# Kernel tuning notes

Measured on AMD Instinct MI355X. Metric: run time of the kernel, lower is better.

## Reference

```python
import jax, jax.numpy as jnp
import numpy as np

N, E, F_IN, H, D, C = 50000, 800000, 128, 4, 64, 40
HD = H * D
NEG_SLOPE = 0.2


def setup_inputs() -> dict:
    key = jax.random.key(0)
    ks = jax.random.split(key, 16)
    x = jax.random.normal(ks[0], (N, F_IN), dtype=jnp.float32)
    edge_index = jax.random.randint(ks[1], (2, E), 0, N, dtype=jnp.int64)
    def glorot(k, shape):
        fan = shape[0] + shape[-1]
        return jax.random.normal(k, shape, dtype=jnp.float32) * jnp.sqrt(2.0 / fan)
    params = {
        'W1': glorot(ks[2], (F_IN, HD)), 'as1': glorot(ks[3], (H, D)), 'ad1': glorot(ks[4], (H, D)), 'b1': jnp.zeros((HD,), jnp.float32),
        'W2': glorot(ks[5], (HD, HD)),   'as2': glorot(ks[6], (H, D)), 'ad2': glorot(ks[7], (H, D)), 'b2': jnp.zeros((HD,), jnp.float32),
        'W3': glorot(ks[8], (HD, HD)),   'as3': glorot(ks[9], (H, D)), 'ad3': glorot(ks[10], (H, D)), 'b3': jnp.zeros((HD,), jnp.float32),
        'Wl': glorot(ks[11], (HD, C)),   'bl': jnp.zeros((C,), jnp.float32),
    }
    return {'x': x, 'edge_index': edge_index, **params}


def gat_layer(x, src, dst, W, a_src, a_dst, b):
    # x: [N, F] -> h: [N, H, D]
    h = (x @ W).reshape(N, H, D)
    alpha_s = jnp.sum(h * a_src, axis=-1)  # [N, H]
    alpha_d = jnp.sum(h * a_dst, axis=-1)  # [N, H]
    e = alpha_s[src] + alpha_d[dst]        # [E', H]
    e = jnp.where(e > 0, e, NEG_SLOPE * e)  # leaky_relu
    # segment softmax over destination nodes
    m = jax.ops.segment_max(e, dst, num_segments=N)  # [N, H]
    m = jnp.where(jnp.isfinite(m), m, 0.0)
    ex = jnp.exp(e - m[dst])
    s = jax.ops.segment_sum(ex, dst, num_segments=N)  # [N, H]
    att = ex / (s[dst] + 1e-16)                        # [E', H]
    # weighted scatter-aggregate of source features
    out = jax.ops.segment_sum(h[src] * att[:, :, None], dst, num_segments=N)  # [N, H, D]
    return out.reshape(N, HD) + b


def reference(x, edge_index, W1, as1, ad1, b1, W2, as2, ad2, b2, W3, as3, ad3, b3, Wl, bl):
    # PyG GATConv adds self-loops by default
    loops = jnp.arange(N, dtype=edge_index.dtype)
    src = jnp.concatenate([edge_index[0], loops])
    dst = jnp.concatenate([edge_index[1], loops])
    # dropout is identity in eval mode
    h = jax.nn.elu(gat_layer(x, src, dst, W1, as1, ad1, b1))
    h = jax.nn.elu(gat_layer(h, src, dst, W2, as2, ad2, b2))
    h = jax.nn.elu(gat_layer(h, src, dst, W3, as3, ad3, b3))
    logits = h @ Wl + bl
    return jax.nn.log_softmax(logits, axis=1)
```

## Files before the change

kernel.cpp:

```cpp
#include <hip/hip_runtime.h>
#include <math.h>

#define NN 50000
#define NE 800000
#define ET (NE + NN)
#define FIN 128
#define HDIM 256
#define NHEAD 4
#define NCLS 40
#define NEG 0.2f
#define NB_SCAN ((NN + 255) / 256)

typedef short bf16x8 __attribute__((ext_vector_type(8)));
typedef float f32x4 __attribute__((ext_vector_type(4)));

__device__ __forceinline__ unsigned short f2b(float f) {
    unsigned int u = __float_as_uint(f);
    unsigned int r = (u + 0x7fffu + ((u >> 16) & 1u)) >> 16;
    return (unsigned short)r;
}
__device__ __forceinline__ float b2f(unsigned short u) {
    unsigned int x = ((unsigned int)u) << 16;
    return __uint_as_float(x);
}

__global__ void detect_kernel(const int* __restrict__ ei32, int* __restrict__ flag) {
    if (threadIdx.x == 0 && blockIdx.x == 0) {
        int is64 = 1;
        for (int i = 1; i < 256; i += 2)
            if (ei32[i] != 0) { is64 = 0; break; }
        *flag = is64;
    }
}

__device__ __forceinline__ int load_node(const int* ei32, int is64, long long idx) {
    return is64 ? ei32[2 * idx] : ei32[idx];
}

__global__ void deg_kernel(const int* __restrict__ ei32, const int* __restrict__ flag,
                           int* __restrict__ deg) {
    int e = blockIdx.x * blockDim.x + threadIdx.x;
    if (e >= ET) return;
    int is64 = *flag;
    int d = (e < NE) ? load_node(ei32, is64, (long long)NE + e) : (e - NE);
    atomicAdd(&deg[d], 1);
}

__global__ void scan1(const int* __restrict__ deg, int* __restrict__ incl,
                      int* __restrict__ bsum) {
    __shared__ int sm[256];
    int i = blockIdx.x * 256 + threadIdx.x;
    int v = (i < NN) ? deg[i] : 0;
    sm[threadIdx.x] = v;
    __syncthreads();
    for (int o = 1; o < 256; o <<= 1) {
        int add = (threadIdx.x >= o) ? sm[threadIdx.x - o] : 0;
        __syncthreads();
        sm[threadIdx.x] += add;
        __syncthreads();
    }
    if (i < NN) incl[i] = sm[threadIdx.x];
    if (threadIdx.x == 255) bsum[blockIdx.x] = sm[255];
}

__global__ void scan2(int* __restrict__ bsum) {
    __shared__ int sm[256];
    int t = threadIdx.x;
    sm[t] = (t < NB_SCAN) ? bsum[t] : 0;
    __syncthreads();
    if (t == 0) {
        int run = 0;
        for (int b = 0; b < NB_SCAN; b++) { int v = sm[b]; sm[b] = run; run += v; }
    }
    __syncthreads();
    if (t < NB_SCAN) bsum[t] = sm[t];
}

__global__ void scan3(const int* __restrict__ incl, const int* __restrict__ bsum,
                      const int* __restrict__ deg, int* __restrict__ indptr,
                      int* __restrict__ cursor) {
    int i = blockIdx.x * 256 + threadIdx.x;
    if (i < NN) {
        int v = bsum[blockIdx.x] + incl[i];
        indptr[i + 1] = v;
        cursor[i] = v - deg[i];
    }
    if (i == 0) indptr[0] = 0;
}

__global__ void fill_kernel(const int* __restrict__ ei32, const int* __restrict__ flag,
                            int* __restrict__ cursor, int* __restrict__ esrc) {
    int e = blockIdx.x * blockDim.x + threadIdx.x;
    if (e >= ET) return;
    int is64 = *flag;
    int s, d;
    if (e < NE) {
        s = load_node(ei32, is64, (long long)e);
        d = load_node(ei32, is64, (long long)NE + e);
    } else {
        s = d = e - NE;
    }
    int pos = atomicAdd(&cursor[d], 1);
    esrc[pos] = s;
}

__global__ __launch_bounds__(256) void conv_kernel(const float* __restrict__ in,
                                                   unsigned short* __restrict__ out, int n) {
    int i = (blockIdx.x * 256 + threadIdx.x) * 8;
    if (i + 8 > n) return;
    float4 f0 = *(const float4*)(in + i);
    float4 f1 = *(const float4*)(in + i + 4);
    ushort4 a, b;
    a.x = f2b(f0.x); a.y = f2b(f0.y); a.z = f2b(f0.z); a.w = f2b(f0.w);
    b.x = f2b(f1.x); b.y = f2b(f1.y); b.z = f2b(f1.z); b.w = f2b(f1.w);
    *(ushort4*)(out + i) = a;
    *(ushort4*)(out + i + 4) = b;
}

__global__ __launch_bounds__(256) void wconv_kernel(const float* __restrict__ W,
                                                    unsigned short* __restrict__ Wt, int K) {
    __shared__ float sm[32][33];
    int tx = threadIdx.x & 31, ty = threadIdx.x >> 5;
    int n0 = blockIdx.x * 32, k0 = blockIdx.y * 32;
#pragma unroll
    for (int j = 0; j < 4; j++)
        sm[ty + j * 8][tx] = W[(size_t)(k0 + ty + j * 8) * HDIM + n0 + tx];
    __syncthreads();
#pragma unroll
    for (int j = 0; j < 4; j++)
        Wt[(size_t)(n0 + ty + j * 8) * K + k0 + tx] = f2b(sm[tx][ty + j * 8]);
}

__global__ __launch_bounds__(256) void gemm_mfma(const unsigned short* __restrict__ A,
                                                 const unsigned short* __restrict__ Bt,
                                                 unsigned short* __restrict__ Cb,
                                                 const float* __restrict__ a_s,
                                                 const float* __restrict__ a_d,
                                                 float* __restrict__ als,
                                                 float* __restrict__ ald,
                                                 int M, int K) {
    __shared__ unsigned short As[128][72];
    __shared__ unsigned short Bs[64][72];
    int t = threadIdx.x;
    int lane = t & 63, wid = t >> 6;
    int r0 = blockIdx.y * 128, n0 = blockIdx.x * 64;

    f32x4 acc[2][4];
#pragma unroll
    for (int m = 0; m < 2; m++)
#pragma unroll
        for (int n = 0; n < 4; n++)
            acc[m][n] = (f32x4){0.f, 0.f, 0.f, 0.f};

    int ar = t >> 1, ah = (t & 1) * 32;
    int arow = r0 + ar; if (arow > M - 1) arow = M - 1;
    const unsigned short* ga = A + (size_t)arow * K + ah;
    int bn = t >> 2, bq = (t & 3) * 16;
    const unsigned short* gb = Bt + (size_t)(n0 + bn) * K + bq;

    int fr = lane & 15;
    int kf = (lane >> 4) * 8;

    for (int k0 = 0; k0 < K; k0 += 64) {
#pragma unroll
        for (int j = 0; j < 4; j++)
            *(uint4*)&As[ar][ah + j * 8] = *(const uint4*)(ga + k0 + j * 8);
#pragma unroll
        for (int j = 0; j < 2; j++)
            *(uint4*)&Bs[bn][bq + j * 8] = *(const uint4*)(gb + k0 + j * 8);
        __syncthreads();
#pragma unroll
        for (int kk = 0; kk < 64; kk += 32) {
            bf16x8 a[2], b[4];
#pragma unroll
            for (int m = 0; m < 2; m++)
                a[m] = *(const bf16x8*)&As[wid * 32 + m * 16 + fr][kk + kf];
#pragma unroll
            for (int n = 0; n < 4; n++)
                b[n] = *(const bf16x8*)&Bs[n * 16 + fr][kk + kf];
#pragma unroll
            for (int m = 0; m < 2; m++)
#pragma unroll
                for (int n = 0; n < 4; n++)
                    acc[m][n] = __builtin_amdgcn_mfma_f32_16x16x32_bf16(a[m], b[n], acc[m][n], 0, 0, 0);
        }
        __syncthreads();
    }

    int rbase = r0 + wid * 32 + (lane >> 4) * 4;
    int cbase = n0 + fr;
    int head = n0 >> 6;
    float asv[4], adv[4];
#pragma unroll
    for (int n = 0; n < 4; n++) {
        asv[n] = a_s[cbase + n * 16];
        adv[n] = a_d[cbase + n * 16];
    }
#pragma unroll
    for (int m = 0; m < 2; m++)
#pragma unroll
        for (int q = 0; q < 4; q++) {
            int gr = rbase + m * 16 + q;
            float vs = 0.f, vd = 0.f;
#pragma unroll
            for (int n = 0; n < 4; n++) {
                float v = acc[m][n][q];
                vs += v * asv[n];
                vd += v * adv[n];
                if (gr < M) Cb[(size_t)gr * HDIM + cbase + n * 16] = f2b(v);
            }
#pragma unroll
            for (int o = 8; o > 0; o >>= 1) {
                vs += __shfl_xor(vs, o);
                vd += __shfl_xor(vd, o);
            }
            if (fr == 0 && gr < M) {
                als[gr * NHEAD + head] = vs;
                ald[gr * NHEAD + head] = vd;
            }
        }
}

__global__ __launch_bounds__(256) void agg_kernel(const unsigned short* __restrict__ projb,
                                                  const float* __restrict__ als,
                                                  const float* __restrict__ ald,
                                                  const int* __restrict__ indptr,
                                                  const int* __restrict__ esrc,
                                                  const float* __restrict__ bias,
                                                  unsigned short* __restrict__ featb) {
    int wid = threadIdx.x >> 6;
    int v = blockIdx.x * 4 + wid;
    if (v >= NN) return;
    int lane = threadIdx.x & 63;
    int h = lane >> 4;
    int sub = lane & 15;
    int beg = indptr[v], end = indptr[v + 1];
    float adv = ald[v * NHEAD + h];

    float m = -INFINITY, ss = 0.f;
    for (int i = beg + sub; i < end; i += 16) {
        int s = esrc[i];
        float e = als[s * NHEAD + h] + adv;
        e = e > 0.f ? e : NEG * e;
        if (e > m) {
            ss = ss * __expf(m - e) + 1.f;
            m = e;
        } else {
            ss += __expf(e - m);
        }
    }
#pragma unroll
    for (int o = 8; o > 0; o >>= 1) {
        float m2 = __shfl_xor(m, o);
        float s2 = __shfl_xor(ss, o);
        float mn = fmaxf(m, m2);
        float a = (m == mn) ? ss : ss * __expf(m - mn);
        float b = (m2 == mn) ? s2 : s2 * __expf(m2 - mn);
        m = mn;
        ss = a + b;
    }
    float inv = 1.f / (ss + 1e-16f);

    float4 acc = make_float4(0.f, 0.f, 0.f, 0.f);
    int c = beg;
    for (; c + 16 <= end; c += 16) {
        int sreg = esrc[c + sub];
        float e = als[sreg * NHEAD + h] + adv;
        e = e > 0.f ? e : NEG * e;
        float wreg = __expf(e - m) * inv;

        ushort4 p[16];
#pragma unroll
        for (int j = 0; j < 16; j++) {
            int s = __shfl(sreg, j);
            p[j] = *(const ushort4*)(projb + (size_t)s * HDIM + (lane << 2));
        }
#pragma unroll
        for (int j = 0; j < 16; j++) {
            float w = __shfl(wreg, (h << 4) | j);
            acc.x += b2f(p[j].x) * w;
            acc.y += b2f(p[j].y) * w;
            acc.z += b2f(p[j].z) * w;
            acc.w += b2f(p[j].w) * w;
        }
    }
    int n = end - c;
    if (n > 0) {
        float wreg = 0.f;
        int sreg = 0;
        if (sub < n) {
            sreg = esrc[c + sub];
            float e = als[sreg * NHEAD + h] + adv;
            e = e > 0.f ? e : NEG * e;
            wreg = __expf(e - m) * inv;
        }
        for (int j = 0; j < n; j++) {
            float w = __shfl(wreg, (h << 4) | j);
            int s = __shfl(sreg, j);
            const ushort4 p = *(const ushort4*)(projb + (size_t)s * HDIM + (lane << 2));
            acc.x += b2f(p.x) * w;
            acc.y += b2f(p.y) * w;
            acc.z += b2f(p.z) * w;
            acc.w += b2f(p.w) * w;
        }
    }

    const float4 b4 = *(const float4*)(bias + (lane << 2));
    float4 r;
    r.x = acc.x + b4.x;
    r.y = acc.y + b4.y;
    r.z = acc.z + b4.z;
    r.w = acc.w + b4.w;
    r.x = r.x > 0.f ? r.x : __expf(r.x) - 1.f;
    r.y = r.y > 0.f ? r.y : __expf(r.y) - 1.f;
    r.z = r.z > 0.f ? r.z : __expf(r.z) - 1.f;
    r.w = r.w > 0.f ? r.w : __expf(r.w) - 1.f;
    ushort4 o4;
    o4.x = f2b(r.x); o4.y = f2b(r.y); o4.z = f2b(r.z); o4.w = f2b(r.w);
    *(ushort4*)(featb + (size_t)v * HDIM + (lane << 2)) = o4;
}

__global__ __launch_bounds__(256) void final_kernel(const unsigned short* __restrict__ featb,
                                                    const float* __restrict__ Wl,
                                                    const float* __restrict__ bl,
                                                    float* __restrict__ out) {
    const int BK = 16;
    __shared__ float As[BK][65];
    __shared__ float Bs[BK][65];
    int tx = threadIdx.x & 15, ty = threadIdx.x >> 4;
    int row0 = blockIdx.x * 64;
    float acc[4][4] = {};
    for (int k0 = 0; k0 < HDIM; k0 += BK) {
#pragma unroll
        for (int i = 0; i < 4; i++) {
            int l = threadIdx.x + 256 * i;
            int r = l >> 4, c = l & 15;
            int gr = row0 + r;
            float v = 0.f;
            if (gr < NN) v = b2f(featb[(size_t)gr * HDIM + k0 + c]);
            As[c][r] = v;
        }
#pragma unroll
        for (int i = 0; i < 4; i++) {
            int l = threadIdx.x + 256 * i;
            int r = l >> 6, c = l & 63;
            Bs[r][c] = (c < NCLS) ? Wl[(size_t)(k0 + r) * NCLS + c] : 0.f;
        }
        __syncthreads();
#pragma unroll
        for (int k = 0; k < BK; k++) {
            float a[4], b[4];
#pragma unroll
            for (int i = 0; i < 4; i++) a[i] = As[k][ty + 16 * i];
#pragma unroll
            for (int j = 0; j < 4; j++) b[j] = Bs[k][tx + 16 * j];
#pragma unroll
            for (int i = 0; i < 4; i++)
#pragma unroll
                for (int j = 0; j < 4; j++) acc[i][j] += a[i] * b[j];
        }
        __syncthreads();
    }
    float b0 = bl[tx], b1 = bl[tx + 16], b2 = (tx < 8) ? bl[tx + 32] : 0.f;
#pragma unroll
    for (int i = 0; i < 4; i++) {
        int gr = row0 + ty + 16 * i;
        if (gr >= NN) continue;
        float l0 = acc[i][0] + b0;
        float l1 = acc[i][1] + b1;
        float l2 = (tx < 8) ? acc[i][2] + b2 : -INFINITY;
        float m = fmaxf(fmaxf(l0, l1), l2);
#pragma unroll
        for (int o = 8; o > 0; o >>= 1) m = fmaxf(m, __shfl_xor(m, o));
        float s = __expf(l0 - m) + __expf(l1 - m) + ((tx < 8) ? __expf(l2 - m) : 0.f);
#pragma unroll
        for (int o = 8; o > 0; o >>= 1) s += __shfl_xor(s, o);
        float lse = m + __logf(s);
        out[(size_t)gr * NCLS + tx] = l0 - lse;
        out[(size_t)gr * NCLS + tx + 16] = l1 - lse;
        if (tx < 8) out[(size_t)gr * NCLS + tx + 32] = l2 - lse;
    }
}

extern "C" void kernel_launch(void* const* d_in, const int* in_sizes, int n_in,
                              void* d_out, int out_size, void* d_ws, size_t ws_size,
                              hipStream_t stream) {
    const float* x  = (const float*)d_in[0];
    const int* ei32 = (const int*)d_in[1];
    const float* W1 = (const float*)d_in[2];
    const float* as1 = (const float*)d_in[3];
    const float* ad1 = (const float*)d_in[4];
    const float* b1 = (const float*)d_in[5];
    const float* W2 = (const float*)d_in[6];
    const float* as2 = (const float*)d_in[7];
    const float* ad2 = (const float*)d_in[8];
    const float* b2 = (const float*)d_in[9];
    const float* W3 = (const float*)d_in[10];
    const float* as3 = (const float*)d_in[11];
    const float* ad3 = (const float*)d_in[12];
    const float* b3 = (const float*)d_in[13];
    const float* Wl = (const float*)d_in[14];
    const float* bl = (const float*)d_in[15];
    float* out = (float*)d_out;

    char* w = (char*)d_ws;
    unsigned short* projb = (unsigned short*)w;  w += (size_t)NN * HDIM * 2;
    unsigned short* featb = (unsigned short*)w;  w += (size_t)NN * HDIM * 2;
    unsigned short* xb    = (unsigned short*)w;  w += (size_t)NN * FIN * 2;
    unsigned short* Wt1b  = (unsigned short*)w;  w += (size_t)HDIM * FIN * 2;
    unsigned short* Wt2b  = (unsigned short*)w;  w += (size_t)HDIM * HDIM * 2;
    unsigned short* Wt3b  = (unsigned short*)w;  w += (size_t)HDIM * HDIM * 2;
    float* als  = (float*)w;  w += (size_t)NN * NHEAD * 4;
    float* ald  = (float*)w;  w += (size_t)NN * NHEAD * 4;
    int* deg    = (int*)w;    w += (size_t)NN * 4;
    int* incl   = (int*)w;    w += (size_t)NN * 4;
    int* bsum   = (int*)w;    w += 256 * 4;
    int* indptr = (int*)w;    w += (size_t)(NN + 1) * 4;
    int* cursor = (int*)w;    w += (size_t)NN * 4;
    int* esrc   = (int*)w;    w += (size_t)ET * 4;
    int* flag   = (int*)w;    w += 64;

    conv_kernel<<<(NN * FIN / 8 + 255) / 256, 256, 0, stream>>>(x, xb, NN * FIN);
    wconv_kernel<<<dim3(8, FIN / 32), 256, 0, stream>>>(W1, Wt1b, FIN);
    wconv_kernel<<<dim3(8, HDIM / 32), 256, 0, stream>>>(W2, Wt2b, HDIM);
    wconv_kernel<<<dim3(8, HDIM / 32), 256, 0, stream>>>(W3, Wt3b, HDIM);

    hipMemsetAsync(deg, 0, (size_t)NN * 4, stream);
    detect_kernel<<<1, 64, 0, stream>>>(ei32, flag);
    deg_kernel<<<(ET + 255) / 256, 256, 0, stream>>>(ei32, flag, deg);
    scan1<<<NB_SCAN, 256, 0, stream>>>(deg, incl, bsum);
    scan2<<<1, 256, 0, stream>>>(bsum);
    scan3<<<NB_SCAN, 256, 0, stream>>>(incl, bsum, deg, indptr, cursor);
    fill_kernel<<<(ET + 255) / 256, 256, 0, stream>>>(ei32, flag, cursor, esrc);

    dim3 ggrid(HDIM / 64, (NN + 127) / 128);
    int agrid = (NN + 3) / 4;

    gemm_mfma<<<ggrid, 256, 0, stream>>>(xb, Wt1b, projb, as1, ad1, als, ald, NN, FIN);
    agg_kernel<<<agrid, 256, 0, stream>>>(projb, als, ald, indptr, esrc, b1, featb);
    gemm_mfma<<<ggrid, 256, 0, stream>>>(featb, Wt2b, projb, as2, ad2, als, ald, NN, HDIM);
    agg_kernel<<<agrid, 256, 0, stream>>>(projb, als, ald, indptr, esrc, b2, featb);
    gemm_mfma<<<ggrid, 256, 0, stream>>>(featb, Wt3b, projb, as3, ad3, als, ald, NN, HDIM);
    agg_kernel<<<agrid, 256, 0, stream>>>(projb, als, ald, indptr, esrc, b3, featb);
    final_kernel<<<(NN + 63) / 64, 256, 0, stream>>>(featb, Wl, bl, out);
}
```

Measured before the change: 479.1 us.

## Fuse input bf16 conversion into GEMM, stage C via LDS, cache edge scores

```diff
diff --git a/kernel.cpp b/kernel.cpp
--- a/kernel.cpp
+++ b/kernel.cpp
@@ -104,19 +104,6 @@
     esrc[pos] = s;
 }
 
-__global__ __launch_bounds__(256) void conv_kernel(const float* __restrict__ in,
-                                                   unsigned short* __restrict__ out, int n) {
-    int i = (blockIdx.x * 256 + threadIdx.x) * 8;
-    if (i + 8 > n) return;
-    float4 f0 = *(const float4*)(in + i);
-    float4 f1 = *(const float4*)(in + i + 4);
-    ushort4 a, b;
-    a.x = f2b(f0.x); a.y = f2b(f0.y); a.z = f2b(f0.z); a.w = f2b(f0.w);
-    b.x = f2b(f1.x); b.y = f2b(f1.y); b.z = f2b(f1.z); b.w = f2b(f1.w);
-    *(ushort4*)(out + i) = a;
-    *(ushort4*)(out + i + 4) = b;
-}
-
 __global__ __launch_bounds__(256) void wconv_kernel(const float* __restrict__ W,
                                                     unsigned short* __restrict__ Wt, int K) {
     __shared__ float sm[32][33];
@@ -132,6 +119,7 @@
 }
 
 __global__ __launch_bounds__(256) void gemm_mfma(const unsigned short* __restrict__ A,
+                                                 const float* __restrict__ A32,
                                                  const unsigned short* __restrict__ Bt,
                                                  unsigned short* __restrict__ Cb,
                                                  const float* __restrict__ a_s,
@@ -155,6 +143,7 @@
     int ar = t >> 1, ah = (t & 1) * 32;
     int arow = r0 + ar; if (arow > M - 1) arow = M - 1;
     const unsigned short* ga = A + (size_t)arow * K + ah;
+    const float* ga32 = A32 ? (A32 + (size_t)arow * K + ah) : (const float*)0;
     int bn = t >> 2, bq = (t & 3) * 16;
     const unsigned short* gb = Bt + (size_t)(n0 + bn) * K + bq;
 
@@ -162,9 +151,23 @@
     int kf = (lane >> 4) * 8;
 
     for (int k0 = 0; k0 < K; k0 += 64) {
-#pragma unroll
-        for (int j = 0; j < 4; j++)
-            *(uint4*)&As[ar][ah + j * 8] = *(const uint4*)(ga + k0 + j * 8);
+        if (A32) {
+#pragma unroll
+            for (int j = 0; j < 4; j++) {
+                float4 fa = *(const float4*)(ga32 + k0 + j * 8);
+                float4 fb = *(const float4*)(ga32 + k0 + j * 8 + 4);
+                union { ushort4 u[2]; uint4 v; } pk;
+                pk.u[0].x = f2b(fa.x); pk.u[0].y = f2b(fa.y);
+                pk.u[0].z = f2b(fa.z); pk.u[0].w = f2b(fa.w);
+                pk.u[1].x = f2b(fb.x); pk.u[1].y = f2b(fb.y);
+                pk.u[1].z = f2b(fb.z); pk.u[1].w = f2b(fb.w);
+                *(uint4*)&As[ar][ah + j * 8] = pk.v;
+            }
+        } else {
+#pragma unroll
+            for (int j = 0; j < 4; j++)
+                *(uint4*)&As[ar][ah + j * 8] = *(const uint4*)(ga + k0 + j * 8);
+        }
 #pragma unroll
         for (int j = 0; j < 2; j++)
             *(uint4*)&Bs[bn][bq + j * 8] = *(const uint4*)(gb + k0 + j * 8);
@@ -207,7 +210,6 @@
                 float v = acc[m][n][q];
                 vs += v * asv[n];
                 vd += v * adv[n];
-                if (gr < M) Cb[(size_t)gr * HDIM + cbase + n * 16] = f2b(v);
             }
 #pragma unroll
             for (int o = 8; o > 0; o >>= 1) {
@@ -219,6 +221,25 @@
                 ald[gr * NHEAD + head] = vd;
             }
         }
+
+    unsigned short (*Cs)[68] = (unsigned short(*)[68])&As[0][0];
+    int lr0 = wid * 32 + (lane >> 4) * 4;
+#pragma unroll
+    for (int m = 0; m < 2; m++)
+#pragma unroll
+        for (int q = 0; q < 4; q++)
+#pragma unroll
+            for (int n = 0; n < 4; n++)
+                Cs[lr0 + m * 16 + q][fr + n * 16] = f2b(acc[m][n][q]);
+    __syncthreads();
+    int tr = t >> 4;
+    int tc = (t & 15) * 4;
+#pragma unroll
+    for (int rr = 0; rr < 8; rr++) {
+        int lr = tr + rr * 16;
+        int gr = r0 + lr;
+        if (gr < M) *(ushort4*)(Cb + (size_t)gr * HDIM + n0 + tc) = *(const ushort4*)&Cs[lr][tc];
+    }
 }
 
 __global__ __launch_bounds__(256) void agg_kernel(const unsigned short* __restrict__ projb,
@@ -237,11 +258,16 @@
     int beg = indptr[v], end = indptr[v + 1];
     float adv = ald[v * NHEAD + h];
 
+    float e0 = 0.f, e1 = 0.f;
+    int s0r = 0, s1r = 0;
     float m = -INFINITY, ss = 0.f;
-    for (int i = beg + sub; i < end; i += 16) {
+    int idx = 0;
+    for (int i = beg + sub; i < end; i += 16, idx++) {
         int s = esrc[i];
         float e = als[s * NHEAD + h] + adv;
         e = e > 0.f ? e : NEG * e;
+        if (idx == 0) { e0 = e; s0r = s; }
+        else if (idx == 1) { e1 = e; s1r = s; }
         if (e > m) {
             ss = ss * __expf(m - e) + 1.f;
             m = e;
@@ -263,11 +289,18 @@
 
     float4 acc = make_float4(0.f, 0.f, 0.f, 0.f);
     int c = beg;
-    for (; c + 16 <= end; c += 16) {
-        int sreg = esrc[c + sub];
-        float e = als[sreg * NHEAD + h] + adv;
-        e = e > 0.f ? e : NEG * e;
-        float wreg = __expf(e - m) * inv;
+    int chunk = 0;
+    for (; c + 16 <= end; c += 16, chunk++) {
+        int sreg;
+        float eC;
+        if (chunk == 0) { sreg = s0r; eC = e0; }
+        else if (chunk == 1) { sreg = s1r; eC = e1; }
+        else {
+            sreg = esrc[c + sub];
+            eC = als[sreg * NHEAD + h] + adv;
+            eC = eC > 0.f ? eC : NEG * eC;
+        }
+        float wreg = __expf(eC - m) * inv;
 
         ushort4 p[16];
 #pragma unroll
@@ -286,14 +319,16 @@
     }
     int n = end - c;
     if (n > 0) {
-        float wreg = 0.f;
-        int sreg = 0;
-        if (sub < n) {
-            sreg = esrc[c + sub];
-            float e = als[sreg * NHEAD + h] + adv;
-            e = e > 0.f ? e : NEG * e;
-            wreg = __expf(e - m) * inv;
-        }
+        int sreg;
+        float eT;
+        if (chunk == 0) { sreg = s0r; eT = e0; }
+        else if (chunk == 1) { sreg = s1r; eT = e1; }
+        else {
+            sreg = (sub < n) ? esrc[c + sub] : 0;
+            eT = als[sreg * NHEAD + h] + adv;
+            eT = eT > 0.f ? eT : NEG * eT;
+        }
+        float wreg = (sub < n) ? __expf(eT - m) * inv : 0.f;
         for (int j = 0; j < n; j++) {
             float w = __shfl(wreg, (h << 4) | j);
             int s = __shfl(sreg, j);
@@ -406,7 +441,6 @@
     char* w = (char*)d_ws;
     unsigned short* projb = (unsigned short*)w;  w += (size_t)NN * HDIM * 2;
     unsigned short* featb = (unsigned short*)w;  w += (size_t)NN * HDIM * 2;
-    unsigned short* xb    = (unsigned short*)w;  w += (size_t)NN * FIN * 2;
     unsigned short* Wt1b  = (unsigned short*)w;  w += (size_t)HDIM * FIN * 2;
     unsigned short* Wt2b  = (unsigned short*)w;  w += (size_t)HDIM * HDIM * 2;
     unsigned short* Wt3b  = (unsigned short*)w;  w += (size_t)HDIM * HDIM * 2;
@@ -420,7 +454,6 @@
     int* esrc   = (int*)w;    w += (size_t)ET * 4;
     int* flag   = (int*)w;    w += 64;
 
-    conv_kernel<<<(NN * FIN / 8 + 255) / 256, 256, 0, stream>>>(x, xb, NN * FIN);
     wconv_kernel<<<dim3(8, FIN / 32), 256, 0, stream>>>(W1, Wt1b, FIN);
     wconv_kernel<<<dim3(8, HDIM / 32), 256, 0, stream>>>(W2, Wt2b, HDIM);
     wconv_kernel<<<dim3(8, HDIM / 32), 256, 0, stream>>>(W3, Wt3b, HDIM);
@@ -436,11 +469,11 @@
     dim3 ggrid(HDIM / 64, (NN + 127) / 128);
     int agrid = (NN + 3) / 4;
 
-    gemm_mfma<<<ggrid, 256, 0, stream>>>(xb, Wt1b, projb, as1, ad1, als, ald, NN, FIN);
+    gemm_mfma<<<ggrid, 256, 0, stream>>>((const unsigned short*)0, x, Wt1b, projb, as1, ad1, als, ald, NN, FIN);
     agg_kernel<<<agrid, 256, 0, stream>>>(projb, als, ald, indptr, esrc, b1, featb);
-    gemm_mfma<<<ggrid, 256, 0, stream>>>(featb, Wt2b, projb, as2, ad2, als, ald, NN, HDIM);
+    gemm_mfma<<<ggrid, 256, 0, stream>>>(featb, (const float*)0, Wt2b, projb, as2, ad2, als, ald, NN, HDIM);
     agg_kernel<<<agrid, 256, 0, stream>>>(projb, als, ald, indptr, esrc, b2, featb);
-    gemm_mfma<<<ggrid, 256, 0, stream>>>(featb, Wt3b, projb, as3, ad3, als, ald, NN, HDIM);
+    gemm_mfma<<<ggrid, 256, 0, stream>>>(featb, (const float*)0, Wt3b, projb, as3, ad3, als, ald, NN, HDIM);
     agg_kernel<<<agrid, 256, 0, stream>>>(projb, als, ald, indptr, esrc, b3, featb);
     final_kernel<<<(NN + 63) / 64, 256, 0, stream>>>(featb, Wl, bl, out);
 }
```

Result: faster. 451.5 us (-5.8%).
